# Performance work log

Measured on AMD Instinct MI355X. Metric: run time of the kernel, lower is better.

## Reference

```python
import jax, jax.numpy as jnp
from jax import lax
import numpy as np

P = 128      # stored adversarial patch resolution
WIN = 256    # max pasted-patch extent (>= max patch_size = sqrt(300*300*0.4) ~ 190)
MINH = 60.0  # min_patch_height
H, W, B, N = 896, 896, 8, 24


def _bilinear(img, ys, xs):
    """Bilinearly sample img [h,w,c] on the grid ys x xs -> [len(ys), len(xs), c]."""
    h, w = img.shape[0], img.shape[1]
    ys = jnp.clip(ys, 0.0, h - 1.0)
    xs = jnp.clip(xs, 0.0, w - 1.0)
    y0 = jnp.floor(ys); x0 = jnp.floor(xs)
    y0i = y0.astype(jnp.int32); x0i = x0.astype(jnp.int32)
    y1i = jnp.minimum(y0i + 1, h - 1); x1i = jnp.minimum(x0i + 1, w - 1)
    wy = (ys - y0)[:, None, None]; wx = (xs - x0)[None, :, None]
    v00 = img[y0i][:, x0i]; v01 = img[y0i][:, x1i]
    v10 = img[y1i][:, x0i]; v11 = img[y1i][:, x1i]
    return (1 - wy) * ((1 - wx) * v00 + wx * v01) + wy * ((1 - wx) * v10 + wx * v11)


def setup_inputs() -> dict:
    key = jax.random.key(0)
    ks = jax.random.split(key, 8)
    ymin = jax.random.uniform(ks[0], (B, N), minval=0.0, maxval=H - 320.0)
    bh = jax.random.uniform(ks[1], (B, N), minval=80.0, maxval=300.0)
    xmin = jax.random.uniform(ks[2], (B, N), minval=0.0, maxval=W - 320.0)
    bw = jax.random.uniform(ks[3], (B, N), minval=80.0, maxval=300.0)
    boxes = jnp.stack([ymin, xmin, ymin + bh, xmin + bw], axis=-1)
    images = jax.random.uniform(ks[4], (B, H, W, 3))
    patch = jax.random.uniform(ks[5], (P, P, 3))
    Ws = jax.random.normal(ks[6], (2, 1)) * 0.5
    bs = jnp.zeros((1,), jnp.float32)
    Wg = jax.random.normal(ks[7], (2, P * P)) * 0.5
    bg = jnp.zeros((P * P,), jnp.float32)
    return {"boxes": boxes, "images": images, "patch": patch,
            "Ws": Ws, "bs": bs, "Wg": Wg, "bg": bg}


def reference(boxes, images, patch, Ws, bs, Wg, bg):
    Bx, Hx, Wx, C = images.shape
    Hf, Wf = float(Hx), float(Wx)
    mu_p = patch.mean((0, 1)); sd_p = patch.std((0, 1)) + 1e-6

    def per_image(image, bxs):
        bh = (bxs[:, 2] - bxs[:, 0]) / Hf
        bw = (bxs[:, 3] - bxs[:, 1]) / Wf
        feats = jnp.stack([bh, bw], axis=-1)                      # [N,2]
        scales = jax.nn.sigmoid(feats @ Ws + bs)[:, 0] * 0.4
        # Patcher.create (vectorized over boxes)
        h = bxs[:, 2] - bxs[:, 0]; w = bxs[:, 3] - bxs[:, 1]
        ps = jnp.floor(jnp.sqrt(h * w * scales))                  # square patch side
        oy = bxs[:, 0] + h / 2.0; ox = bxs[:, 1] + w / 2.0
        ymp = jnp.maximum(oy - ps / 2.0, 0.0)
        xmp = jnp.maximum(ox - ps / 2.0, 0.0)
        ymp = jnp.where(ymp + ps > Hf, Hf - ps, ymp)
        xmp = jnp.where(xmp + ps > Wf, Wf - ps, xmp)
        pboxes = jnp.stack([ymp, xmp, ps, ps], axis=-1)           # [N,4]
        valid = ps > MINH                                          # filter-by-mask
        masks = jax.nn.sigmoid(feats @ Wg + bg).reshape(-1, P, P, 1)  # gen masks
        img_p = jnp.pad(image, ((0, WIN), (0, WIN), (0, 0)))

        def body(carry, inp):
            imgc, bgl = carry
            pbox, mask, vld = inp
            yi = pbox[0].astype(jnp.int32); xi = pbox[1].astype(jnp.int32)
            ph = pbox[2].astype(jnp.int32); pw = pbox[3].astype(jnp.int32)
            phf = jnp.maximum(ph, 1).astype(jnp.float32)
            pwf = jnp.maximum(pw, 1).astype(jnp.float32)
            # crop background region -> fixed PxP
            ys = yi.astype(jnp.float32) + (jnp.arange(P, dtype=jnp.float32) + 0.5) * phf / P - 0.5
            xs = xi.astype(jnp.float32) + (jnp.arange(P, dtype=jnp.float32) + 0.5) * pwf / P - 0.5
            patch_bg = _bilinear(imgc, ys, xs)                    # [P,P,C]
            # histogram (moment) matching of patch to local background
            mu_b = patch_bg.mean((0, 1)); sd_b = patch_bg.std((0, 1)) + 1e-6
            matched = (patch - mu_p) / sd_p * sd_b + mu_b
            blended = jnp.where(mask > 0.5, matched, patch_bg)
            r = jnp.arange(WIN, dtype=jnp.float32)
            sy = (r + 0.5) * P / phf - 0.5
            sx = (r + 0.5) * P / pwf - 0.5
            im_win = _bilinear(blended, sy, sx)
            win = lax.dynamic_slice(imgc, (yi, xi, 0), (WIN, WIN, imgc.shape[-1]))
            inside = (jnp.arange(WIN)[:, None] < ph) & (jnp.arange(WIN)[None, :] < pw) & vld
            upd = jnp.where(inside[..., None], im_win, win)
            imgc = lax.dynamic_update_slice(imgc, upd, (yi, xi, 0))
            bgl = bgl + jnp.where(vld, mask.mean(), 0.0)          # generator.bg_loss
            return (imgc, bgl), None

        (img_p, bgl), _ = lax.scan(body, (img_p, jnp.zeros((), jnp.float32)),
                                   (pboxes, masks, valid))
        # scale loss over valid boxes: mean + 0.5*variance
        vf = valid.astype(jnp.float32)
        n = jnp.maximum(vf.sum(), 1.0)
        m = (scales * vf).sum() / n
        var = (vf * (scales - m) ** 2).sum() / n
        return img_p[:Hx, :Wx], bgl + m + 0.5 * var

    out, losses = jax.vmap(per_image)(images, boxes)
    return out, losses.sum()
```

## Files before the change

kernel.cpp:

```cpp
#include <hip/hip_runtime.h>

#define PPX  128
#define PP2  16384
#define IMH  896
#define IMW  896
#define NB   24
#define NI   8
#define HP   1152
#define WP   1152
#define MAXG 6
#define NMB  (NI*NB)
#define NCPY 2048
#define M1   12

#define WS_BOX  8
#define WS_MASK 2048
#define WS_SCH  100352
#define WS_LIST 100608
#define WS_MSUM 101760
#define WS_PART 103424
#define WS_PBG  140288

__device__ __forceinline__ void box_geom(const float* __restrict__ bx,
    const float* __restrict__ Wsc, const float* __restrict__ bsc,
    float& scale, float& ps, int& yi, int& xi, int& ph, int& vld)
{
  float ya=bx[0], xa=bx[1], yb=bx[2], xb=bx[3];
  float bh=(yb-ya)/(float)IMH, bw=(xb-xa)/(float)IMW;
  float z = bh*Wsc[0]+bw*Wsc[1]+bsc[0];
  float sig = 1.f/(1.f+expf(-z));
  scale = sig*0.4f;
  float h=yb-ya, w=xb-xa;
  ps = floorf(sqrtf((h*w)*scale));
  float oy=ya+h*0.5f, ox=xa+w*0.5f;
  float ymp=fmaxf(oy-ps*0.5f,0.f), xmp=fmaxf(ox-ps*0.5f,0.f);
  if (ymp+ps>(float)IMH) ymp=(float)IMH-ps;
  if (xmp+ps>(float)IMW) xmp=(float)IMW-ps;
  yi=(int)ymp; xi=(int)xmp; ph=(int)ps;
  vld = (ps>60.f) ? 1 : 0;
}

__device__ __forceinline__ void analytic3(int rr, int cc, float phf,
    const float* __restrict__ pbg1, const float* __restrict__ patch,
    const unsigned* msk, const float* ab, float v[3])
{
  float sy = ((rr + 0.5f)*128.0f)/phf - 0.5f;
  float sx = ((cc + 0.5f)*128.0f)/phf - 0.5f;
  sy = fminf(fmaxf(sy, 0.f), 127.f);
  sx = fminf(fmaxf(sx, 0.f), 127.f);
  float fy0 = floorf(sy), fx0 = floorf(sx);
  int py0 = (int)fy0, px0 = (int)fx0;
  int py1 = py0 + 1 < 127 ? py0 + 1 : 127;
  int px1 = px0 + 1 < 127 ? px0 + 1 : 127;
  float wy = sy - fy0, wx = sx - fx0;
  int i00 = (py0<<7)+px0, i01 = (py0<<7)+px1, i10 = (py1<<7)+px0, i11 = (py1<<7)+px1;
  bool m00 = (msk[i00>>5] >> (i00&31)) & 1u;
  bool m01 = (msk[i01>>5] >> (i01&31)) & 1u;
  bool m10 = (msk[i10>>5] >> (i10&31)) & 1u;
  bool m11 = (msk[i11>>5] >> (i11&31)) & 1u;
  #pragma unroll
  for (int ch = 0; ch < 3; ++ch) {
    float a = ab[ch], be = ab[3+ch];
    float t00 = m00 ? patch[i00*3+ch]*a + be : pbg1[i00*3+ch];
    float t01 = m01 ? patch[i01*3+ch]*a + be : pbg1[i01*3+ch];
    float t10 = m10 ? patch[i10*3+ch]*a + be : pbg1[i10*3+ch];
    float t11 = m11 ? patch[i11*3+ch]*a + be : pbg1[i11*3+ch];
    v[ch] = (1.f-wy)*((1.f-wx)*t00 + wx*t01) + wy*((1.f-wx)*t10 + wx*t11);
  }
}

__device__ __forceinline__ void crop_plain(
    const float* __restrict__ src, float* __restrict__ ws, int b, int n, int blk,
    float (*s_red)[6])
{
  const int tid = threadIdx.x;
  const int* bi = (const int*)(ws + WS_BOX + (b*NB + n)*8);
  const int yi = bi[2], xi = bi[3], ph = bi[4];
  const float phf = (float)(ph > 1 ? ph : 1);
  float* __restrict__ pbg = ws + WS_PBG + (size_t)(b*NB + n)*PP2*3;
  float sm[3] = {0,0,0}, sq[3] = {0,0,0};
  #pragma unroll
  for (int k = 0; k < 2; ++k) {
    int idx = blk*512 + k*256 + tid;
    int py = idx >> 7, px = idx & 127;
    float ys = ((float)yi + (py + 0.5f)*phf*(1.0f/PPX)) - 0.5f;
    float xs = ((float)xi + (px + 0.5f)*phf*(1.0f/PPX)) - 0.5f;
    ys = fminf(fmaxf(ys, 0.f), (float)(HP-1));
    xs = fminf(fmaxf(xs, 0.f), (float)(WP-1));
    float fy0 = floorf(ys), fx0 = floorf(xs);
    int y0 = (int)fy0, x0 = (int)fx0;
    int y1 = y0 + 1 < HP-1 ? y0 + 1 : HP-1;
    int x1 = x0 + 1 < WP-1 ? x0 + 1 : WP-1;
    float wy = ys - fy0, wx = xs - fx0;
    bool y0i = y0 < IMH, y1i = y1 < IMH, x0i = x0 < IMW, x1i = x1 < IMW;
    const float* r0 = src + (size_t)y0*IMW*3;
    const float* r1 = src + (size_t)y1*IMW*3;
    #pragma unroll
    for (int c = 0; c < 3; ++c) {
      float v00 = (y0i && x0i) ? r0[x0*3+c] : 0.f;
      float v01 = (y0i && x1i) ? r0[x1*3+c] : 0.f;
      float v10 = (y1i && x0i) ? r1[x0*3+c] : 0.f;
      float v11 = (y1i && x1i) ? r1[x1*3+c] : 0.f;
      float v = (1.f-wy)*((1.f-wx)*v00 + wx*v01) + wy*((1.f-wx)*v10 + wx*v11);
      pbg[idx*3+c] = v;
      sm[c] += v; sq[c] += v*v;
    }
  }
  float vals[6] = {sm[0],sm[1],sm[2],sq[0],sq[1],sq[2]};
  #pragma unroll
  for (int off = 32; off; off >>= 1)
    #pragma unroll
    for (int k = 0; k < 6; ++k) vals[k] += __shfl_down(vals[k], off);
  int wid = tid >> 6;
  __syncthreads();
  if ((tid & 63) == 0)
    for (int k = 0; k < 6; ++k) s_red[wid][k] = vals[k];
  __syncthreads();
  if (tid == 0) {
    float* part = ws + WS_PART + (size_t)((b*NB + n)*32 + blk)*6;
    for (int k = 0; k < 6; ++k)
      part[k] = s_red[0][k] + s_red[1][k] + s_red[2][k] + s_red[3][k];
  }
}

__global__ __launch_bounds__(256) void first_k(
    float* __restrict__ out, const float* __restrict__ images,
    const float* __restrict__ boxes,
    const float* __restrict__ Wsc, const float* __restrict__ bsc,
    const float* __restrict__ Wg, const float* __restrict__ bgv,
    const float* __restrict__ patch, float* __restrict__ ws)
{
  const int bid = blockIdx.x, tid = threadIdx.x;
  if (bid == NCPY) {
    __shared__ float s_red6[256][6];
    float s0=0,s1=0,s2=0,q0=0,q1=0,q2=0;
    for (int i = tid; i < PP2; i += 256) {
      float a = patch[i*3+0], b = patch[i*3+1], c = patch[i*3+2];
      s0+=a; s1+=b; s2+=c; q0+=a*a; q1+=b*b; q2+=c*c;
    }
    s_red6[tid][0]=s0; s_red6[tid][1]=s1; s_red6[tid][2]=s2;
    s_red6[tid][3]=q0; s_red6[tid][4]=q1; s_red6[tid][5]=q2;
    __syncthreads();
    for (int s = 128; s > 0; s >>= 1) {
      if (tid < s)
        for (int k=0;k<6;++k) s_red6[tid][k] += s_red6[tid+s][k];
      __syncthreads();
    }
    if (tid == 0) {
      for (int c=0;c<3;++c) {
        float mu  = s_red6[0][c]   * (1.0f/PP2);
        float var = s_red6[0][3+c] * (1.0f/PP2) - mu*mu;
        float sd  = sqrtf(fmaxf(var, 0.f)) + 1e-6f;
        ws[c] = mu; ws[3+c] = sd;
      }
    }
    return;
  }
  if (bid == NCPY + 1) {
    __shared__ int g_yi[NI*NB], g_xi[NI*NB], g_ph[NI*NB], g_vl[NI*NB];
    if (tid < NI*NB) {
      float scale, ps; int yi, xi, ph, vld;
      box_geom(boxes + tid*4, Wsc, bsc, scale, ps, yi, xi, ph, vld);
      g_yi[tid]=yi; g_xi[tid]=xi; g_ph[tid]=ph; g_vl[tid]=vld;
      float* bst = ws + WS_BOX + tid*8;
      bst[0] = scale;
      bst[1] = ps;
      ((int*)bst)[2] = yi;
      ((int*)bst)[3] = xi;
      ((int*)bst)[4] = ph;
      bst[5] = vld ? 1.f : 0.f;
    }
    __syncthreads();
    if (tid < NI) {
      unsigned* sch = ((unsigned*)ws) + WS_SCH + tid*32;
      unsigned* lst = ((unsigned*)ws) + WS_LIST + tid*(MAXG*NB);
      int lv[NB];
      int cnt[MAXG];
      for (int L = 0; L < MAXG; ++L) cnt[L] = 0;
      for (int n = 0; n < NB; ++n) {
        int idx = tid*NB + n;
        if (!g_vl[idx]) { lv[n] = -1; sch[n] = 255u; continue; }
        int y0 = g_yi[idx]-2, y1 = g_yi[idx]+g_ph[idx]+3;
        int x0 = g_xi[idx]-2, x1 = g_xi[idx]+g_ph[idx]+3;
        int L = 0;
        for (int m = 0; m < n; ++m) {
          if (lv[m] < 0) continue;
          int mi = tid*NB + m;
          int my0 = g_yi[mi]-2, my1 = g_yi[mi]+g_ph[mi]+3;
          int mx0 = g_xi[mi]-2, mx1 = g_xi[mi]+g_ph[mi]+3;
          if (y0 < my1 && my0 < y1 && x0 < mx1 && mx0 < x1)
            L = max(L, lv[m] + 1);
        }
        lv[n] = L;
        sch[n] = (unsigned)L;
        if (L < MAXG) lst[L*NB + cnt[L]++] = (unsigned)n;
      }
      for (int L = 0; L < MAXG; ++L) sch[24 + L] = (unsigned)cnt[L];
    }
    return;
  }

  if (bid < NMB*8) {
    const int bn = bid >> 3, q = bid & 7;
    float bh = (boxes[bn*4+2]-boxes[bn*4+0])/(float)IMH;
    float bw = (boxes[bn*4+3]-boxes[bn*4+1])/(float)IMW;
    unsigned* mwords = ((unsigned*)ws) + WS_MASK + bn*512;
    float lsum = 0.f;
    const int lane = tid & 63;
    #pragma unroll
    for (int i = 0; i < 8; ++i) {
      int p = q*2048 + i*256 + tid;
      float zz = bh*Wg[p] + bw*Wg[PP2 + p] + bgv[p];
      lsum += 1.0f / (1.0f + expf(-zz));
      unsigned long long m = __ballot(zz > 0.0f);
      if (lane == 0) {
        int base = p >> 5;
        mwords[base]   = (unsigned)(m & 0xffffffffULL);
        mwords[base+1] = (unsigned)(m >> 32);
      }
    }
    #pragma unroll
    for (int off = 32; off; off >>= 1) lsum += __shfl_down(lsum, off);
    __shared__ float s_r[4];
    if ((tid & 63) == 0) s_r[tid >> 6] = lsum;
    __syncthreads();
    if (tid == 0) ws[WS_MSUM + bn*8 + q] = s_r[0] + s_r[1] + s_r[2] + s_r[3];
  }

  {
    const float4* src4 = (const float4*)images;
    float4* dst4 = (float4*)out;
    const int n4 = NI*IMH*IMW*3/4;
    for (int i = bid*256 + tid; i < n4; i += NCPY*256) dst4[i] = src4[i];
  }
}

__global__ __launch_bounds__(256) void crop_k(
    float* __restrict__ out, const float* __restrict__ images,
    float* __restrict__ ws, int L, int M)
{
  const int bid = blockIdx.x, tid = threadIdx.x;
  const int b = bid / (M*32);
  const int rem = bid - b*(M*32);
  const int j = rem >> 5, blk = rem & 31;
  __shared__ float s_red[4][6];
  __shared__ int s_cn[NB];
  __shared__ int s_cc;
  const unsigned* sch = ((const unsigned*)ws) + WS_SCH + b*32;
  if (tid == 0) s_cc = (int)sch[24 + L];
  __syncthreads();
  const int cc = s_cc;
  if (j >= cc) return;
  if (tid < cc) s_cn[tid] = (int)(((const unsigned*)ws) + WS_LIST + b*(MAXG*NB))[L*NB + tid];
  __syncthreads();
  const float* src = (L == 0) ? images + (size_t)b*IMH*IMW*3
                              : out + (size_t)b*IMH*IMW*3;
  for (int jj = j; jj < cc; jj += M)
    crop_plain(src, ws, b, s_cn[jj], blk, s_red);
}

__global__ __launch_bounds__(256) void paste_k(
    float* __restrict__ out, const float* __restrict__ patch,
    float* __restrict__ ws, int L, int M)
{
  const int bid = blockIdx.x, tid = threadIdx.x;
  if (bid >= NI*M*32) {
    __shared__ float l_sc[NI*NB], l_ms[NI*NB], l_vl[NI*NB];
    if (tid < NI*NB) {
      const float* bst = ws + WS_BOX + tid*8;
      l_sc[tid] = bst[0]; l_vl[tid] = bst[5];
      float ms = 0.f;
      for (int q = 0; q < 8; ++q) ms += ws[WS_MSUM + tid*8 + q];
      l_ms[tid] = ms;
    }
    __syncthreads();
    if (tid == 0) {
      float total = 0.f;
      for (int b = 0; b < NI; ++b) {
        float sum_s = 0.f, cnt = 0.f, bgl = 0.f;
        for (int n = 0; n < NB; ++n) {
          int idx = b*NB + n;
          float v = l_vl[idx];
          sum_s += l_sc[idx]*v; cnt += v; bgl += (l_ms[idx]*(1.0f/PP2))*v;
        }
        float nn = fmaxf(cnt, 1.0f);
        float m = sum_s / nn;
        float var = 0.f;
        for (int n = 0; n < NB; ++n) {
          int idx = b*NB + n;
          float d = l_sc[idx] - m;
          var += l_vl[idx]*d*d;
        }
        var /= nn;
        total += bgl + m + 0.5f*var;
      }
      out[(size_t)NI*IMH*IMW*3] = total;
    }
    return;
  }
  const int b = bid / (M*32);
  const int rem = bid - b*(M*32);
  const int j = rem >> 5, r = rem & 31;
  __shared__ int s_cp;
  __shared__ int s_pn[NB];
  __shared__ float s_ab[6];
  __shared__ unsigned s_mask[512];
  const unsigned* sch = ((const unsigned*)ws) + WS_SCH + b*32;
  if (tid == 0) s_cp = (int)sch[24 + L];
  __syncthreads();
  const int cp = s_cp;
  if (j >= cp) return;
  if (tid < cp) s_pn[tid] = (int)(((const unsigned*)ws) + WS_LIST + b*(MAXG*NB))[L*NB + tid];
  __syncthreads();
  float* __restrict__ img = out + (size_t)b*IMH*IMW*3;

  for (int jj = j; jj < cp; jj += M) {
    const int n = s_pn[jj];
    if (tid < 32) {
      const float* part = ws + WS_PART + (size_t)((b*NB + n)*32 + tid)*6;
      float v[6];
      #pragma unroll
      for (int k = 0; k < 6; ++k) v[k] = part[k];
      #pragma unroll
      for (int off = 16; off; off >>= 1)
        #pragma unroll
        for (int k = 0; k < 6; ++k) v[k] += __shfl_down(v[k], off, 32);
      if (tid == 0) {
        #pragma unroll
        for (int c = 0; c < 3; ++c) {
          float mu  = v[c]   * (1.0f/PP2);
          float var = v[3+c] * (1.0f/PP2) - mu*mu;
          float sd  = sqrtf(fmaxf(var, 0.f)) + 1e-6f;
          float alpha = sd / ws[3+c];
          s_ab[c]   = alpha;
          s_ab[3+c] = mu - ws[c]*alpha;
        }
      }
    }
    {
      const unsigned* mwords = ((const unsigned*)ws) + WS_MASK + (b*NB + n)*512;
      s_mask[tid]       = mwords[tid];
      s_mask[tid + 256] = mwords[tid + 256];
    }
    __syncthreads();
    const int* bi = (const int*)(ws + WS_BOX + (b*NB + n)*8);
    const int yi = bi[2], xi = bi[3], ph = bi[4];
    const float phf = (float)(ph > 1 ? ph : 1);
    const float* pbgp = ws + WS_PBG + (size_t)(b*NB + n)*PP2*3;
    const int tot = ph*ph;
    const int chunk = (tot + 31) / 32;
    const int i0 = r*chunk;
    const int i1 = min(tot, i0 + chunk);
    for (int idx = i0 + tid; idx < i1; idx += 256) {
      int rr = (int)((unsigned)idx / (unsigned)ph);
      int cx = idx - rr*ph;
      float v[3];
      analytic3(rr, cx, phf, pbgp, patch, s_mask, s_ab, v);
      float* dst = img + ((size_t)(yi + rr)*IMW + (xi + cx))*3;
      dst[0] = v[0]; dst[1] = v[1]; dst[2] = v[2];
    }
    __syncthreads();
  }
}

__global__ __launch_bounds__(1024) void fb_k(
    float* __restrict__ out, const float* __restrict__ patch, float* __restrict__ ws)
{
  const int b = blockIdx.x, tid = threadIdx.x;
  const unsigned* sch = ((const unsigned*)ws) + WS_SCH + b*32;
  __shared__ float s_red[16][6];
  __shared__ float s_ab[6];
  __shared__ unsigned s_mask[512];
  float* __restrict__ img = out + (size_t)b*IMH*IMW*3;

  for (int n = 0; n < NB; ++n) {
    unsigned g = sch[n];
    if (g < (unsigned)MAXG || g == 255u) continue;
    const int* bi = (const int*)(ws + WS_BOX + (b*NB + n)*8);
    const int yi = bi[2], xi = bi[3], ph = bi[4];
    const float phf = (float)(ph > 1 ? ph : 1);
    float* __restrict__ pbg = ws + WS_PBG + (size_t)(b*NB + n)*PP2*3;

    float sm[3]={0,0,0}, sq[3]={0,0,0};
    #pragma unroll
    for (int k = 0; k < PP2/1024; ++k) {
      int idx = k*1024 + tid;
      int py = idx >> 7, px = idx & 127;
      float ys = ((float)yi + (py + 0.5f)*phf*(1.0f/PPX)) - 0.5f;
      float xs = ((float)xi + (px + 0.5f)*phf*(1.0f/PPX)) - 0.5f;
      ys = fminf(fmaxf(ys, 0.f), (float)(HP-1));
      xs = fminf(fmaxf(xs, 0.f), (float)(WP-1));
      float fy0 = floorf(ys), fx0 = floorf(xs);
      int y0 = (int)fy0, x0 = (int)fx0;
      int y1 = y0 + 1 < HP-1 ? y0 + 1 : HP-1;
      int x1 = x0 + 1 < WP-1 ? x0 + 1 : WP-1;
      float wy = ys - fy0, wx = xs - fx0;
      bool y0i = y0 < IMH, y1i = y1 < IMH, x0i = x0 < IMW, x1i = x1 < IMW;
      const float* r0 = img + (size_t)y0*IMW*3;
      const float* r1 = img + (size_t)y1*IMW*3;
      #pragma unroll
      for (int c = 0; c < 3; ++c) {
        float v00 = (y0i && x0i) ? r0[x0*3+c] : 0.f;
        float v01 = (y0i && x1i) ? r0[x1*3+c] : 0.f;
        float v10 = (y1i && x0i) ? r1[x0*3+c] : 0.f;
        float v11 = (y1i && x1i) ? r1[x1*3+c] : 0.f;
        float v = (1.f-wy)*((1.f-wx)*v00 + wx*v01) + wy*((1.f-wx)*v10 + wx*v11);
        pbg[idx*3+c] = v;
        sm[c] += v; sq[c] += v*v;
      }
    }
    float vals[6] = {sm[0],sm[1],sm[2],sq[0],sq[1],sq[2]};
    #pragma unroll
    for (int off = 32; off; off >>= 1)
      #pragma unroll
      for (int k = 0; k < 6; ++k) vals[k] += __shfl_down(vals[k], off);
    if ((tid & 63) == 0)
      for (int k = 0; k < 6; ++k) s_red[tid >> 6][k] = vals[k];
    if (tid < 512) {
      const unsigned* mwords = ((const unsigned*)ws) + WS_MASK + (b*NB + n)*512;
      s_mask[tid] = mwords[tid];
    }
    __syncthreads();
    if (tid == 0) {
      float acc[6] = {0,0,0,0,0,0};
      for (int w2 = 0; w2 < 16; ++w2)
        for (int k = 0; k < 6; ++k) acc[k] += s_red[w2][k];
      for (int c = 0; c < 3; ++c) {
        float mu  = acc[c]   * (1.0f/PP2);
        float var = acc[3+c] * (1.0f/PP2) - mu*mu;
        float sd  = sqrtf(fmaxf(var, 0.f)) + 1e-6f;
        float alpha = sd / ws[3+c];
        s_ab[c]   = alpha;
        s_ab[3+c] = mu - ws[c]*alpha;
      }
    }
    __syncthreads();
    const int tot = ph*ph;
    for (int idx = tid; idx < tot; idx += 1024) {
      int rr = (int)((unsigned)idx / (unsigned)ph);
      int cc = idx - rr*ph;
      float v[3];
      analytic3(rr, cc, phf, pbg, patch, s_mask, s_ab, v);
      float* dst = img + ((size_t)(yi + rr)*IMW + (xi + cc))*3;
      dst[0] = v[0]; dst[1] = v[1]; dst[2] = v[2];
    }
    __syncthreads();
  }
}

extern "C" void kernel_launch(void* const* d_in, const int* in_sizes, int n_in,
                              void* d_out, int out_size, void* d_ws, size_t ws_size,
                              hipStream_t stream) {
  const float* boxes  = (const float*)d_in[0];
  const float* images = (const float*)d_in[1];
  const float* patch  = (const float*)d_in[2];
  const float* Wsc    = (const float*)d_in[3];
  const float* bsc    = (const float*)d_in[4];
  const float* Wg     = (const float*)d_in[5];
  const float* bgv    = (const float*)d_in[6];
  float* out = (float*)d_out;
  float* ws  = (float*)d_ws;

  first_k<<<NCPY + 2, 256, 0, stream>>>(out, images, boxes, Wsc, bsc, Wg, bgv, patch, ws);
  crop_k <<<NI*M1*32, 256, 0, stream>>>(out, images, ws, 0, M1);
  paste_k<<<NI*M1*32 + 1, 256, 0, stream>>>(out, patch, ws, 0, M1);
  crop_k <<<NI*8*32, 256, 0, stream>>>(out, images, ws, 1, 8);
  paste_k<<<NI*8*32, 256, 0, stream>>>(out, patch, ws, 1, 8);
  crop_k <<<NI*4*32, 256, 0, stream>>>(out, images, ws, 2, 4);
  paste_k<<<NI*4*32, 256, 0, stream>>>(out, patch, ws, 2, 4);
  crop_k <<<NI*2*32, 256, 0, stream>>>(out, images, ws, 3, 2);
  paste_k<<<NI*2*32, 256, 0, stream>>>(out, patch, ws, 3, 2);
  crop_k <<<NI*2*32, 256, 0, stream>>>(out, images, ws, 4, 2);
  paste_k<<<NI*2*32, 256, 0, stream>>>(out, patch, ws, 4, 2);
  crop_k <<<NI*2*32, 256, 0, stream>>>(out, images, ws, 5, 2);
  paste_k<<<NI*2*32, 256, 0, stream>>>(out, patch, ws, 5, 2);
  fb_k<<<NI, 1024, 0, stream>>>(out, patch, ws);
}
```

Measured before the change: 177.0 us.

## Fuse level-0 crop into first kernel with per-block box geometry recompute

```diff
diff --git a/kernel.cpp b/kernel.cpp
--- a/kernel.cpp
+++ b/kernel.cpp
@@ -11,6 +11,7 @@
 #define MAXG 6
 #define NMB  (NI*NB)
 #define NCPY 2048
+#define NCR0 (NI*NB*32)
 #define M1   12
 
 #define WS_BOX  8
@@ -69,13 +70,11 @@
   }
 }
 
-__device__ __forceinline__ void crop_plain(
-    const float* __restrict__ src, float* __restrict__ ws, int b, int n, int blk,
-    float (*s_red)[6])
+__device__ __forceinline__ void crop_geom(
+    const float* __restrict__ src, float* __restrict__ ws, int b, int n,
+    int yi, int xi, int ph, int blk, float (*s_red)[6])
 {
   const int tid = threadIdx.x;
-  const int* bi = (const int*)(ws + WS_BOX + (b*NB + n)*8);
-  const int yi = bi[2], xi = bi[3], ph = bi[4];
   const float phf = (float)(ph > 1 ? ph : 1);
   float* __restrict__ pbg = ws + WS_PBG + (size_t)(b*NB + n)*PP2*3;
   float sm[3] = {0,0,0}, sq[3] = {0,0,0};
@@ -131,7 +130,79 @@
     const float* __restrict__ patch, float* __restrict__ ws)
 {
   const int bid = blockIdx.x, tid = threadIdx.x;
-  if (bid == NCPY) {
+
+  if (bid < NCPY) {
+    const float4* src4 = (const float4*)images;
+    float4* dst4 = (float4*)out;
+    const int n4 = NI*IMH*IMW*3/4;
+    for (int i = bid*256 + tid; i < n4; i += NCPY*256) dst4[i] = src4[i];
+    return;
+  }
+
+  if (bid < NCPY + NMB*8) {
+    const int w = bid - NCPY;
+    const int bn = w >> 3, q = w & 7;
+    float bh = (boxes[bn*4+2]-boxes[bn*4+0])/(float)IMH;
+    float bw = (boxes[bn*4+3]-boxes[bn*4+1])/(float)IMW;
+    unsigned* mwords = ((unsigned*)ws) + WS_MASK + bn*512;
+    float lsum = 0.f;
+    const int lane = tid & 63;
+    #pragma unroll
+    for (int i = 0; i < 8; ++i) {
+      int p = q*2048 + i*256 + tid;
+      float zz = bh*Wg[p] + bw*Wg[PP2 + p] + bgv[p];
+      lsum += 1.0f / (1.0f + expf(-zz));
+      unsigned long long m = __ballot(zz > 0.0f);
+      if (lane == 0) {
+        int base = p >> 5;
+        mwords[base]   = (unsigned)(m & 0xffffffffULL);
+        mwords[base+1] = (unsigned)(m >> 32);
+      }
+    }
+    #pragma unroll
+    for (int off = 32; off; off >>= 1) lsum += __shfl_down(lsum, off);
+    __shared__ float s_r[4];
+    if ((tid & 63) == 0) s_r[tid >> 6] = lsum;
+    __syncthreads();
+    if (tid == 0) ws[WS_MSUM + bn*8 + q] = s_r[0] + s_r[1] + s_r[2] + s_r[3];
+    return;
+  }
+
+  if (bid < NCPY + NMB*8 + NCR0) {
+    const int w = bid - NCPY - NMB*8;
+    const int b = w / (NB*32);
+    const int rem = w - b*(NB*32);
+    const int n = rem >> 5, blk = rem & 31;
+    __shared__ int s_yi[NB], s_xi[NB], s_ph[NB], s_vl[NB];
+    __shared__ int s_ok;
+    __shared__ float s_red[4][6];
+    if (tid < NB) {
+      float scale, ps; int yi, xi, ph, vld;
+      box_geom(boxes + (b*NB + tid)*4, Wsc, bsc, scale, ps, yi, xi, ph, vld);
+      s_yi[tid]=yi; s_xi[tid]=xi; s_ph[tid]=ph; s_vl[tid]=vld;
+    }
+    __syncthreads();
+    if (tid == 0) {
+      int ok = s_vl[n];
+      if (ok) {
+        int y0=s_yi[n]-2, y1=s_yi[n]+s_ph[n]+3;
+        int x0=s_xi[n]-2, x1=s_xi[n]+s_ph[n]+3;
+        for (int m = 0; m < n; ++m) {
+          if (!s_vl[m]) continue;
+          int my0=s_yi[m]-2, my1=s_yi[m]+s_ph[m]+3;
+          int mx0=s_xi[m]-2, mx1=s_xi[m]+s_ph[m]+3;
+          if (y0<my1 && my0<y1 && x0<mx1 && mx0<x1) { ok = 0; break; }
+        }
+      }
+      s_ok = ok;
+    }
+    __syncthreads();
+    if (!s_ok) return;
+    crop_geom(images + (size_t)b*IMH*IMW*3, ws, b, n, s_yi[n], s_xi[n], s_ph[n], blk, s_red);
+    return;
+  }
+
+  if (bid == NCPY + NMB*8 + NCR0) {
     __shared__ float s_red6[256][6];
     float s0=0,s1=0,s2=0,q0=0,q1=0,q2=0;
     for (int i = tid; i < PP2; i += 256) {
@@ -156,7 +227,8 @@
     }
     return;
   }
-  if (bid == NCPY + 1) {
+
+  {
     __shared__ int g_yi[NI*NB], g_xi[NI*NB], g_ph[NI*NB], g_vl[NI*NB];
     if (tid < NI*NB) {
       float scale, ps; int yi, xi, ph, vld;
@@ -197,47 +269,11 @@
       }
       for (int L = 0; L < MAXG; ++L) sch[24 + L] = (unsigned)cnt[L];
     }
-    return;
-  }
-
-  if (bid < NMB*8) {
-    const int bn = bid >> 3, q = bid & 7;
-    float bh = (boxes[bn*4+2]-boxes[bn*4+0])/(float)IMH;
-    float bw = (boxes[bn*4+3]-boxes[bn*4+1])/(float)IMW;
-    unsigned* mwords = ((unsigned*)ws) + WS_MASK + bn*512;
-    float lsum = 0.f;
-    const int lane = tid & 63;
-    #pragma unroll
-    for (int i = 0; i < 8; ++i) {
-      int p = q*2048 + i*256 + tid;
-      float zz = bh*Wg[p] + bw*Wg[PP2 + p] + bgv[p];
-      lsum += 1.0f / (1.0f + expf(-zz));
-      unsigned long long m = __ballot(zz > 0.0f);
-      if (lane == 0) {
-        int base = p >> 5;
-        mwords[base]   = (unsigned)(m & 0xffffffffULL);
-        mwords[base+1] = (unsigned)(m >> 32);
-      }
-    }
-    #pragma unroll
-    for (int off = 32; off; off >>= 1) lsum += __shfl_down(lsum, off);
-    __shared__ float s_r[4];
-    if ((tid & 63) == 0) s_r[tid >> 6] = lsum;
-    __syncthreads();
-    if (tid == 0) ws[WS_MSUM + bn*8 + q] = s_r[0] + s_r[1] + s_r[2] + s_r[3];
-  }
-
-  {
-    const float4* src4 = (const float4*)images;
-    float4* dst4 = (float4*)out;
-    const int n4 = NI*IMH*IMW*3/4;
-    for (int i = bid*256 + tid; i < n4; i += NCPY*256) dst4[i] = src4[i];
   }
 }
 
 __global__ __launch_bounds__(256) void crop_k(
-    float* __restrict__ out, const float* __restrict__ images,
-    float* __restrict__ ws, int L, int M)
+    float* __restrict__ out, float* __restrict__ ws, int L, int M)
 {
   const int bid = blockIdx.x, tid = threadIdx.x;
   const int b = bid / (M*32);
@@ -253,10 +289,12 @@
   if (j >= cc) return;
   if (tid < cc) s_cn[tid] = (int)(((const unsigned*)ws) + WS_LIST + b*(MAXG*NB))[L*NB + tid];
   __syncthreads();
-  const float* src = (L == 0) ? images + (size_t)b*IMH*IMW*3
-                              : out + (size_t)b*IMH*IMW*3;
-  for (int jj = j; jj < cc; jj += M)
-    crop_plain(src, ws, b, s_cn[jj], blk, s_red);
+  const float* src = out + (size_t)b*IMH*IMW*3;
+  for (int jj = j; jj < cc; jj += M) {
+    const int n = s_cn[jj];
+    const int* bi = (const int*)(ws + WS_BOX + (b*NB + n)*8);
+    crop_geom(src, ws, b, n, bi[2], bi[3], bi[4], blk, s_red);
+  }
 }
 
 __global__ __launch_bounds__(256) void paste_k(
@@ -461,18 +499,18 @@
   float* out = (float*)d_out;
   float* ws  = (float*)d_ws;
 
-  first_k<<<NCPY + 2, 256, 0, stream>>>(out, images, boxes, Wsc, bsc, Wg, bgv, patch, ws);
-  crop_k <<<NI*M1*32, 256, 0, stream>>>(out, images, ws, 0, M1);
+  first_k<<<NCPY + NMB*8 + NCR0 + 2, 256, 0, stream>>>(
+      out, images, boxes, Wsc, bsc, Wg, bgv, patch, ws);
   paste_k<<<NI*M1*32 + 1, 256, 0, stream>>>(out, patch, ws, 0, M1);
-  crop_k <<<NI*8*32, 256, 0, stream>>>(out, images, ws, 1, 8);
+  crop_k <<<NI*8*32, 256, 0, stream>>>(out, ws, 1, 8);
   paste_k<<<NI*8*32, 256, 0, stream>>>(out, patch, ws, 1, 8);
-  crop_k <<<NI*4*32, 256, 0, stream>>>(out, images, ws, 2, 4);
+  crop_k <<<NI*4*32, 256, 0, stream>>>(out, ws, 2, 4);
   paste_k<<<NI*4*32, 256, 0, stream>>>(out, patch, ws, 2, 4);
-  crop_k <<<NI*2*32, 256, 0, stream>>>(out, images, ws, 3, 2);
+  crop_k <<<NI*2*32, 256, 0, stream>>>(out, ws, 3, 2);
   paste_k<<<NI*2*32, 256, 0, stream>>>(out, patch, ws, 3, 2);
-  crop_k <<<NI*2*32, 256, 0, stream>>>(out, images, ws, 4, 2);
+  crop_k <<<NI*2*32, 256, 0, stream>>>(out, ws, 4, 2);
   paste_k<<<NI*2*32, 256, 0, stream>>>(out, patch, ws, 4, 2);
-  crop_k <<<NI*2*32, 256, 0, stream>>>(out, images, ws, 5, 2);
+  crop_k <<<NI*2*32, 256, 0, stream>>>(out, ws, 5, 2);
   paste_k<<<NI*2*32, 256, 0, stream>>>(out, patch, ws, 5, 2);
   fb_k<<<NI, 1024, 0, stream>>>(out, patch, ws);
 }
```

Result: slower. 181.3 us (+2.4%).
